# Performance work log

Measured on AMD Instinct MI355X. Metric: run time of the kernel, lower is better.

The kernel has to match this reference:

```python
import jax, jax.numpy as jnp
import numpy as np

MARGIN_POS = 0.0
MARGIN_NEG = 1.0
NUM_CLASSES = 1000


def setup_inputs() -> dict:
    key = jax.random.key(0)
    k1, k2, k3, k4, k5 = jax.random.split(key, 5)
    B, D, M = 1024, 512, 32768
    R = M - B  # memory bank length after dedup/truncate
    embeddings = jax.random.normal(k1, (B, D), dtype=jnp.float32)
    labels = jax.random.randint(k2, (B,), 0, NUM_CLASSES).astype(jnp.int64)
    emb_mem = jax.random.normal(k3, (R, D), dtype=jnp.float32)
    # offset so memory labels are disjoint from batch labels (torch.isin dedup is a no-op)
    lbl_mem = (jax.random.randint(k4, (R,), 0, NUM_CLASSES) + NUM_CLASSES).astype(jnp.int64)
    add_to_mem = jax.random.randint(k5, (B,), 0, 2).astype(bool)
    return {"embeddings": embeddings, "labels": labels, "emb_mem": emb_mem,
            "lbl_mem": lbl_mem, "add_to_mem": add_to_mem}


def _loss(embeddings, labels, emb_mem, lbl_mem):
    B = embeddings.shape[0]
    # reference set = detached batch embeddings ++ memory bank (both are constants w.r.t. grad)
    ref_e = jax.lax.stop_gradient(jnp.concatenate([embeddings, emb_mem], axis=0))  # [R, D]
    ref_l = jnp.concatenate([labels, lbl_mem], axis=0)                              # [R]
    idx_ref = jnp.concatenate([jnp.arange(B, dtype=labels.dtype),
                               -jnp.ones(lbl_mem.shape[0], dtype=labels.dtype)])    # [R]
    # squared L2 distance matrix [B, R] via (|a|^2 + |b|^2 - 2 a.b), clamped at 0
    sq_a = jnp.sum(embeddings * embeddings, axis=1)  # [B]
    sq_b = jnp.sum(ref_e * ref_e, axis=1)            # [R]
    d = jnp.maximum(sq_a[:, None] + sq_b[None, :] - 2.0 * (embeddings @ ref_e.T), 0.0)
    not_self = idx_ref[None, :] != jnp.arange(B, dtype=labels.dtype)[:, None]  # [B, R]
    same = labels[:, None] == ref_l[None, :]                                   # [B, R]
    loss_ap = d - MARGIN_POS
    loss_an = jnp.maximum(MARGIN_NEG - d, 0.0)
    mask_pos = same & not_self & (loss_ap > 0)
    mask_neg = (~same) & not_self & (loss_an > 0)
    eps = 1e-6
    loss_pos = (jnp.where(mask_pos, loss_ap, 0.0).sum(1)
                / (mask_pos.sum(1).astype(d.dtype) + eps)).sum()
    loss_neg = (jnp.where(mask_neg, loss_an, 0.0).sum(1)
                / (mask_neg.sum(1).astype(d.dtype) + eps)).sum()
    return (loss_pos + loss_neg) / B


def reference(embeddings, labels, emb_mem, lbl_mem, add_to_mem):
    # add_to_mem only affects the (stateful) memory-bank update, not the returned loss
    return _loss(embeddings, labels, emb_mem, lbl_mem)
```

## Files before the change

kernel.cpp:

```cpp
#include <hip/hip_runtime.h>

typedef __attribute__((ext_vector_type(8))) short short8;
typedef __attribute__((ext_vector_type(4))) float f32x4;

#define GLOAD16(g, l)                                                        \
  __builtin_amdgcn_global_load_lds(                                          \
      (const __attribute__((address_space(1))) unsigned int*)(g),            \
      (__attribute__((address_space(3))) unsigned int*)(l), 16, 0, 0)

__device__ __forceinline__ unsigned short f2bf(float f) {
  union { float f; unsigned int u; } v;
  v.f = f;
  unsigned int u = v.u;
  u += 0x7FFFu + ((u >> 16) & 1u);
  return (unsigned short)(u >> 16);
}

__device__ __forceinline__ short8 pack8(float4 a, float4 b) {
  short8 r;
  r[0] = (short)f2bf(a.x); r[1] = (short)f2bf(a.y);
  r[2] = (short)f2bf(a.z); r[3] = (short)f2bf(a.w);
  r[4] = (short)f2bf(b.x); r[5] = (short)f2bf(b.y);
  r[6] = (short)f2bf(b.z); r[7] = (short)f2bf(b.w);
  return r;
}

#define BM 128
#define BN 128
#define BK 32

__global__ __launch_bounds__(256)
void prep2_kernel(const float* __restrict__ emb, const int* __restrict__ labels,
                  const float* __restrict__ emb_mem, const int* __restrict__ lbl_mem,
                  unsigned short* __restrict__ refbf, float* __restrict__ sqb,
                  int* __restrict__ reflab, float* __restrict__ facc,
                  int* __restrict__ fcnt, int Bn, int Dn, int Mn) {
  if (blockIdx.x == 0 && threadIdx.x == 0) { *facc = 0.f; *fcnt = 0; }
  int wid = threadIdx.x >> 6, lane = threadIdx.x & 63;
  int row = blockIdx.x * 4 + wid;
  if (row >= Mn) return;
  const float* src = (row < Bn) ? (emb + (size_t)row * Dn)
                                : (emb_mem + (size_t)(row - Bn) * Dn);
  unsigned short* dst = refbf + (size_t)row * Dn;
  float s = 0.f;
  for (int c0 = lane * 8; c0 < Dn; c0 += 64 * 8) {
    float4 v0 = ((const float4*)(src + c0))[0];
    float4 v1 = ((const float4*)(src + c0))[1];
    s += v0.x * v0.x + v0.y * v0.y + v0.z * v0.z + v0.w * v0.w;
    s += v1.x * v1.x + v1.y * v1.y + v1.z * v1.z + v1.w * v1.w;
    *(short8*)(dst + c0) = pack8(v0, v1);
  }
#pragma unroll
  for (int off = 32; off; off >>= 1) s += __shfl_xor(s, off);
  if (lane == 0) {
    sqb[row] = s;
    reflab[row] = (row < Bn) ? labels[row] : lbl_mem[row - Bn];
  }
}

__global__ __launch_bounds__(256)
void gemm512_kernel(const unsigned short* __restrict__ refbf,
                    const float* __restrict__ sqb,
                    const int* __restrict__ reflab,
                    float* __restrict__ part) {
  __shared__ __align__(16) char smem[32768];
  unsigned short* As = (unsigned short*)smem;
  unsigned short* Bs = (unsigned short*)(smem + 8192);
  f32x4* red4 = (f32x4*)smem;

  const int ntiles = 256;
  int bid = blockIdx.x;
  int c = bid & 7, g = bid >> 3;
  int jt = c * 32 + (g >> 3);
  int it = g & 7;
  int rowBase = it * BM, colBase = jt * BN;

  int tid = threadIdx.x, lane = tid & 63, w = tid >> 6;
  int wr = w >> 1, wc = w & 1;
  int l16 = lane & 15, quad = lane >> 4;
  int lrow = lane >> 2, lk = lane & 3;
  int r0 = w * 32 + lrow;
  int ca = (lk - (r0 >> 1)) & 3;

  const char* gA0 = (const char*)refbf + (size_t)(rowBase + r0) * 1024 + ca * 16;
  const char* gA1 = gA0 + 16 * 1024;
  const char* gB0 = (const char*)refbf + (size_t)(colBase + r0) * 1024 + ca * 16;
  const char* gB1 = gB0 + 16 * 1024;
  char* lA = (char*)As + w * 2048;
  char* lB = (char*)Bs + w * 2048;

  f32x4 acc[4][4] = {};
#pragma unroll
  for (int kk = 0; kk < 16; ++kk) {
    GLOAD16(gA0 + kk * 64, lA);
    GLOAD16(gA1 + kk * 64, lA + 1024);
    GLOAD16(gB0 + kk * 64, lB);
    GLOAD16(gB1 + kk * 64, lB + 1024);
    __syncthreads();
    short8 af[4], bfr[4];
#pragma unroll
    for (int mi = 0; mi < 4; ++mi) {
      int row = wr * 64 + mi * 16 + l16;
      af[mi] = *(const short8*)&As[row * BK + ((quad + (row >> 1)) & 3) * 8];
    }
#pragma unroll
    for (int ni = 0; ni < 4; ++ni) {
      int row = wc * 64 + ni * 16 + l16;
      bfr[ni] = *(const short8*)&Bs[row * BK + ((quad + (row >> 1)) & 3) * 8];
    }
#pragma unroll
    for (int mi = 0; mi < 4; ++mi)
#pragma unroll
      for (int ni = 0; ni < 4; ++ni)
        acc[mi][ni] = __builtin_amdgcn_mfma_f32_16x16x32_bf16(
            af[mi], bfr[ni], acc[mi][ni], 0, 0, 0);
    __syncthreads();
  }

  float sqc[4];
  int labc[4];
#pragma unroll
  for (int ni = 0; ni < 4; ++ni) {
    int gcol = colBase + wc * 64 + ni * 16 + l16;
    sqc[ni] = sqb[gcol];
    labc[ni] = reflab[gcol];
  }
#pragma unroll
  for (int mi = 0; mi < 4; ++mi) {
    int lr0 = wr * 64 + mi * 16 + quad * 4;
#pragma unroll
    for (int r = 0; r < 4; ++r) {
      int lrl = lr0 + r;
      int grow = rowBase + lrl;
      float sqr = sqb[grow];
      int labr = reflab[grow];
      float ps = 0.f, ns = 0.f, cpk = 0.f;
#pragma unroll
      for (int ni = 0; ni < 4; ++ni) {
        int gcol = colBase + wc * 64 + ni * 16 + l16;
        float dist = fmaxf(sqr + sqc[ni] - 2.0f * acc[mi][ni][r], 0.f);
        bool self = (gcol == grow);
        bool same = (labc[ni] == labr);
        if (same && !self && dist > 0.f) { ps += dist; cpk += 1.f; }
        if (!same && !self && dist < 1.f) { ns += 1.f - dist; cpk += 512.f; }
      }
      ps += __shfl_xor(ps, 8);
      ns += __shfl_xor(ns, 8);
      cpk += __shfl_xor(cpk, 8);
      if (l16 < 8) {
        f32x4 v = {ps, ns, cpk, 0.f};
        red4[(wc * BM + lrl) * 8 + l16] = v;
      }
    }
  }
  __syncthreads();
  if (tid < BM) {
    f32x4 s = {0.f, 0.f, 0.f, 0.f};
#pragma unroll
    for (int c2 = 0; c2 < 2; ++c2)
#pragma unroll
      for (int k = 0; k < 8; ++k)
        s += red4[(c2 * BM + tid) * 8 + ((k + tid) & 7)];
    float nc = floorf(s[2] * (1.0f / 512.0f));
    float pc = s[2] - 512.f * nc;
    f32x4 o = {s[0], pc, s[1], nc};
    ((f32x4*)part)[(size_t)(rowBase + tid) * ntiles + jt] = o;
  }
}

__global__ __launch_bounds__(256)
void gemm_generic_kernel(const unsigned short* __restrict__ refbf,
                         const float* __restrict__ sqb,
                         const int* __restrict__ reflab,
                         float* __restrict__ part,
                         int Dn, int mtiles, int ntiles) {
  __shared__ unsigned short As[BM * BK];
  __shared__ unsigned short Bs[BN * BK];
  __shared__ f32x4 redbuf4[2 * BM];

  int bid = blockIdx.x;
  int it = bid % mtiles, jt = bid / mtiles;
  int rowBase = it * BM, colBase = jt * BN;
  int tid = threadIdx.x, lane = tid & 63, w = tid >> 6;
  int wr = w >> 1, wc = w & 1;
  int l16 = lane & 15, quad = lane >> 4;
  int lrow = lane >> 2, lk = lane & 3;
  size_t rowB = (size_t)Dn * 2;
  int r0 = w * 32 + lrow;
  int ca = (lk - (r0 >> 1)) & 3;
  const char* gA0 = (const char*)refbf + (size_t)(rowBase + r0) * rowB + ca * 16;
  const char* gA1 = gA0 + 16 * rowB;
  const char* gB0 = (const char*)refbf + (size_t)(colBase + r0) * rowB + ca * 16;
  const char* gB1 = gB0 + 16 * rowB;
  char* lA = (char*)As + w * 2048;
  char* lB = (char*)Bs + w * 2048;

  f32x4 acc[4][4] = {};
  for (int k0 = 0; k0 < Dn; k0 += BK) {
    int koff = k0 * 2;
    GLOAD16(gA0 + koff, lA);
    GLOAD16(gA1 + koff, lA + 1024);
    GLOAD16(gB0 + koff, lB);
    GLOAD16(gB1 + koff, lB + 1024);
    __syncthreads();
    short8 af[4], bfr[4];
#pragma unroll
    for (int mi = 0; mi < 4; ++mi) {
      int row = wr * 64 + mi * 16 + l16;
      af[mi] = *(const short8*)&As[row * BK + ((quad + (row >> 1)) & 3) * 8];
    }
#pragma unroll
    for (int ni = 0; ni < 4; ++ni) {
      int row = wc * 64 + ni * 16 + l16;
      bfr[ni] = *(const short8*)&Bs[row * BK + ((quad + (row >> 1)) & 3) * 8];
    }
#pragma unroll
    for (int mi = 0; mi < 4; ++mi)
#pragma unroll
      for (int ni = 0; ni < 4; ++ni)
        acc[mi][ni] = __builtin_amdgcn_mfma_f32_16x16x32_bf16(
            af[mi], bfr[ni], acc[mi][ni], 0, 0, 0);
    __syncthreads();
  }

  float sqc[4];
  int labc[4];
#pragma unroll
  for (int ni = 0; ni < 4; ++ni) {
    int gcol = colBase + wc * 64 + ni * 16 + l16;
    sqc[ni] = sqb[gcol];
    labc[ni] = reflab[gcol];
  }
#pragma unroll
  for (int mi = 0; mi < 4; ++mi) {
    int lr0 = wr * 64 + mi * 16 + quad * 4;
#pragma unroll
    for (int r = 0; r < 4; ++r) {
      int lrl = lr0 + r;
      int grow = rowBase + lrl;
      float sqr = sqb[grow];
      int labr = reflab[grow];
      float ps = 0.f, pc = 0.f, ns = 0.f, nc = 0.f;
#pragma unroll
      for (int ni = 0; ni < 4; ++ni) {
        int gcol = colBase + wc * 64 + ni * 16 + l16;
        float dist = fmaxf(sqr + sqc[ni] - 2.0f * acc[mi][ni][r], 0.f);
        bool self = (gcol == grow);
        bool same = (labc[ni] == labr);
        if (same && !self && dist > 0.f) { ps += dist; pc += 1.f; }
        if (!same && !self && dist < 1.f) { ns += 1.f - dist; nc += 1.f; }
      }
#pragma unroll
      for (int off = 8; off; off >>= 1) {
        ps += __shfl_xor(ps, off);
        pc += __shfl_xor(pc, off);
        ns += __shfl_xor(ns, off);
        nc += __shfl_xor(nc, off);
      }
      if (l16 == 0) {
        f32x4 v = {ps, pc, ns, nc};
        redbuf4[wc * BM + lrl] = v;
      }
    }
  }
  __syncthreads();
  if (tid < BM) {
    f32x4 s = redbuf4[tid] + redbuf4[BM + tid];
    ((f32x4*)part)[(size_t)(rowBase + tid) * ntiles + jt] = s;
  }
}

__global__ __launch_bounds__(256)
void reduce_final_kernel(const float* __restrict__ part,
                         float* __restrict__ facc, int* __restrict__ fcnt,
                         float* __restrict__ out, int Bn, int ntiles) {
  __shared__ float rsum[4];
  int tid = threadIdx.x, w = tid >> 6, lane = tid & 63;
  int row = blockIdx.x * 4 + w;
  const f32x4* part4 = (const f32x4*)part;
  float rl = 0.f;
  if (row < Bn) {
    f32x4 a = {0.f, 0.f, 0.f, 0.f};
    for (int j = lane; j < ntiles; j += 64)
      a += part4[(size_t)row * ntiles + j];
#pragma unroll
    for (int off = 32; off; off >>= 1) {
      a[0] += __shfl_xor(a[0], off);
      a[1] += __shfl_xor(a[1], off);
      a[2] += __shfl_xor(a[2], off);
      a[3] += __shfl_xor(a[3], off);
    }
    rl = a[0] / (a[1] + 1e-6f) + a[2] / (a[3] + 1e-6f);
  }
  if (lane == 0) rsum[w] = rl;
  __syncthreads();
  if (tid == 0) {
    float bs = rsum[0] + rsum[1] + rsum[2] + rsum[3];
    atomicAdd(facc, bs);
    __threadfence();
    int old = atomicAdd(fcnt, 1);
    if (old == (int)gridDim.x - 1) {
      __threadfence();
      float tot = atomicAdd(facc, 0.f);
      out[0] = tot / (float)Bn;
    }
  }
}

extern "C" void kernel_launch(void* const* d_in, const int* in_sizes, int n_in,
                              void* d_out, int out_size, void* d_ws, size_t ws_size,
                              hipStream_t stream) {
  const float* emb     = (const float*)d_in[0];
  const int*   labels  = (const int*)d_in[1];
  const float* emb_mem = (const float*)d_in[2];
  const int*   lbl_mem = (const int*)d_in[3];

  int Bn = in_sizes[1];
  int Dn = in_sizes[0] / Bn;
  int Rn = in_sizes[3];
  int Mn = Bn + Rn;
  int mtiles = Bn / BM, ntiles = Mn / BN;

  char* ws = (char*)d_ws;
  unsigned short* refbf = (unsigned short*)ws;
  size_t off = (size_t)Mn * Dn * 2;
  float* sqb    = (float*)(ws + off);
  int*   reflab = (int*)(ws + off + (size_t)Mn * 4);
  float* part   = (float*)(ws + off + (size_t)Mn * 8);
  float* facc   = part + (size_t)Bn * ntiles * 4;
  int*   fcnt   = (int*)(facc + 1);

  prep2_kernel<<<(Mn + 3) / 4, 256, 0, stream>>>(
      emb, labels, emb_mem, lbl_mem, refbf, sqb, reflab, facc, fcnt, Bn, Dn, Mn);

  if (Dn == 512 && mtiles == 8 && ntiles == 256) {
    gemm512_kernel<<<2048, 256, 0, stream>>>(refbf, sqb, reflab, part);
  } else {
    gemm_generic_kernel<<<mtiles * ntiles, 256, 0, stream>>>(
        refbf, sqb, reflab, part, Dn, mtiles, ntiles);
  }

  reduce_final_kernel<<<(Bn + 3) / 4, 256, 0, stream>>>(
      part, facc, fcnt, (float*)d_out, Bn, ntiles);
}
```

Measured before the change: 164.0 us.

## Load GEMM fragments directly from global into registers with double buffering

The 512-dim GEMM kernel no longer stages A/B tiles through LDS with global_load_lds and two barriers per k-step. Each lane now loads its MFMA fragments straight from global memory into registers, prefetching the next k-slice while the current one feeds the MFMAs, and launch bounds request 3 blocks per CU. This removes the LDS round-trip and the barriers. In exchange every wave re-reads shared rows from global/L2 with no intra-block reuse, and register pressure goes up.

```diff
diff --git a/kernel.cpp b/kernel.cpp
--- a/kernel.cpp
+++ b/kernel.cpp
@@ -58,15 +58,12 @@
   }
 }
 
-__global__ __launch_bounds__(256)
-void gemm512_kernel(const unsigned short* __restrict__ refbf,
-                    const float* __restrict__ sqb,
-                    const int* __restrict__ reflab,
-                    float* __restrict__ part) {
-  __shared__ __align__(16) char smem[32768];
-  unsigned short* As = (unsigned short*)smem;
-  unsigned short* Bs = (unsigned short*)(smem + 8192);
-  f32x4* red4 = (f32x4*)smem;
+__global__ __launch_bounds__(256, 3)
+void gemm512r_kernel(const unsigned short* __restrict__ refbf,
+                     const float* __restrict__ sqb,
+                     const int* __restrict__ reflab,
+                     float* __restrict__ part) {
+  __shared__ f32x4 red4[2 * BM * 8];
 
   const int ntiles = 256;
   int bid = blockIdx.x;
@@ -78,43 +75,41 @@
   int tid = threadIdx.x, lane = tid & 63, w = tid >> 6;
   int wr = w >> 1, wc = w & 1;
   int l16 = lane & 15, quad = lane >> 4;
-  int lrow = lane >> 2, lk = lane & 3;
-  int r0 = w * 32 + lrow;
-  int ca = (lk - (r0 >> 1)) & 3;
-
-  const char* gA0 = (const char*)refbf + (size_t)(rowBase + r0) * 1024 + ca * 16;
-  const char* gA1 = gA0 + 16 * 1024;
-  const char* gB0 = (const char*)refbf + (size_t)(colBase + r0) * 1024 + ca * 16;
-  const char* gB1 = gB0 + 16 * 1024;
-  char* lA = (char*)As + w * 2048;
-  char* lB = (char*)Bs + w * 2048;
+
+  const char* aP[4];
+  const char* bP[4];
+#pragma unroll
+  for (int mi = 0; mi < 4; ++mi)
+    aP[mi] = (const char*)refbf +
+             (size_t)(rowBase + wr * 64 + mi * 16 + l16) * 1024 + quad * 16;
+#pragma unroll
+  for (int ni = 0; ni < 4; ++ni)
+    bP[ni] = (const char*)refbf +
+             (size_t)(colBase + wc * 64 + ni * 16 + l16) * 1024 + quad * 16;
 
   f32x4 acc[4][4] = {};
+  short8 af[2][4], bfr[2][4];
+#pragma unroll
+  for (int mi = 0; mi < 4; ++mi) af[0][mi] = *(const short8*)(aP[mi]);
+#pragma unroll
+  for (int ni = 0; ni < 4; ++ni) bfr[0][ni] = *(const short8*)(bP[ni]);
+
 #pragma unroll
   for (int kk = 0; kk < 16; ++kk) {
-    GLOAD16(gA0 + kk * 64, lA);
-    GLOAD16(gA1 + kk * 64, lA + 1024);
-    GLOAD16(gB0 + kk * 64, lB);
-    GLOAD16(gB1 + kk * 64, lB + 1024);
-    __syncthreads();
-    short8 af[4], bfr[4];
-#pragma unroll
-    for (int mi = 0; mi < 4; ++mi) {
-      int row = wr * 64 + mi * 16 + l16;
-      af[mi] = *(const short8*)&As[row * BK + ((quad + (row >> 1)) & 3) * 8];
-    }
-#pragma unroll
-    for (int ni = 0; ni < 4; ++ni) {
-      int row = wc * 64 + ni * 16 + l16;
-      bfr[ni] = *(const short8*)&Bs[row * BK + ((quad + (row >> 1)) & 3) * 8];
+    int cur = kk & 1, nxt = cur ^ 1;
+    if (kk < 15) {
+      int ko = (kk + 1) * 64;
+#pragma unroll
+      for (int mi = 0; mi < 4; ++mi) af[nxt][mi] = *(const short8*)(aP[mi] + ko);
+#pragma unroll
+      for (int ni = 0; ni < 4; ++ni) bfr[nxt][ni] = *(const short8*)(bP[ni] + ko);
     }
 #pragma unroll
     for (int mi = 0; mi < 4; ++mi)
 #pragma unroll
       for (int ni = 0; ni < 4; ++ni)
         acc[mi][ni] = __builtin_amdgcn_mfma_f32_16x16x32_bf16(
-            af[mi], bfr[ni], acc[mi][ni], 0, 0, 0);
-    __syncthreads();
+            af[cur][mi], bfr[cur][ni], acc[mi][ni], 0, 0, 0);
   }
 
   float sqc[4];
@@ -334,7 +329,7 @@
       emb, labels, emb_mem, lbl_mem, refbf, sqb, reflab, facc, fcnt, Bn, Dn, Mn);
 
   if (Dn == 512 && mtiles == 8 && ntiles == 256) {
-    gemm512_kernel<<<2048, 256, 0, stream>>>(refbf, sqb, reflab, part);
+    gemm512r_kernel<<<2048, 256, 0, stream>>>(refbf, sqb, reflab, part);
   } else {
     gemm_generic_kernel<<<mtiles * ntiles, 256, 0, stream>>>(
         refbf, sqb, reflab, part, Dn, mtiles, ntiles);
```

Result: slower. 242.6 us (+47.9%).

## Fuse prep, GEMM and reduction into one cooperative persistent kernel

Applied to the files above, without the earlier changes.

Replaces the three separate launches (bf16 convert/norms, distance GEMM with masked partial sums, final reduction) with one cooperative kernel of 512 persistent blocks. The phases are separated by grid-wide syncs, and each block loops over rows and GEMM tiles. This removes launch overhead and inter-kernel gaps. In exchange it adds grid-sync costs, loses the oversubscribed 2048-block GEMM grid, and keeps the three-kernel path as a fallback if the cooperative launch fails.

```diff
diff --git a/kernel.cpp b/kernel.cpp
--- a/kernel.cpp
+++ b/kernel.cpp
@@ -1,4 +1,7 @@
 #include <hip/hip_runtime.h>
+#include <hip/hip_cooperative_groups.h>
+
+namespace cg = cooperative_groups;
 
 typedef __attribute__((ext_vector_type(8))) short short8;
 typedef __attribute__((ext_vector_type(4))) float f32x4;
@@ -28,6 +31,180 @@
 #define BM 128
 #define BN 128
 #define BK 32
+
+__global__ __launch_bounds__(256, 2)
+void fused512_kernel(const float* __restrict__ emb, const int* __restrict__ labels,
+                     const float* __restrict__ emb_mem, const int* __restrict__ lbl_mem,
+                     unsigned short* __restrict__ refbf, float* __restrict__ sqb,
+                     int* __restrict__ reflab, float* __restrict__ part,
+                     float* __restrict__ rowloss, float* __restrict__ out,
+                     int Bn, int Mn) {
+  __shared__ __align__(16) char smem[32768];
+  unsigned short* As = (unsigned short*)smem;
+  unsigned short* Bs = (unsigned short*)(smem + 8192);
+  f32x4* red4 = (f32x4*)smem;
+
+  cg::grid_group grid = cg::this_grid();
+  const int Dn = 512, ntiles = 256;
+  int tid = threadIdx.x, lane = tid & 63, w = tid >> 6;
+  int bid = blockIdx.x, G = gridDim.x;
+
+  for (int row = bid * 4 + w; row < Mn; row += G * 4) {
+    const float* src = (row < Bn) ? (emb + (size_t)row * Dn)
+                                  : (emb_mem + (size_t)(row - Bn) * Dn);
+    unsigned short* dst = refbf + (size_t)row * Dn;
+    float s = 0.f;
+    {
+      int c0 = lane * 8;
+      float4 v0 = ((const float4*)(src + c0))[0];
+      float4 v1 = ((const float4*)(src + c0))[1];
+      s += v0.x * v0.x + v0.y * v0.y + v0.z * v0.z + v0.w * v0.w;
+      s += v1.x * v1.x + v1.y * v1.y + v1.z * v1.z + v1.w * v1.w;
+      *(short8*)(dst + c0) = pack8(v0, v1);
+    }
+#pragma unroll
+    for (int off = 32; off; off >>= 1) s += __shfl_xor(s, off);
+    if (lane == 0) {
+      sqb[row] = s;
+      reflab[row] = (row < Bn) ? labels[row] : lbl_mem[row - Bn];
+    }
+  }
+  __threadfence();
+  grid.sync();
+
+  int wr = w >> 1, wc = w & 1;
+  int l16 = lane & 15, quad = lane >> 4;
+  int lrow = lane >> 2, lk = lane & 3;
+  int sr0 = w * 32 + lrow;
+  int ca = (lk - (sr0 >> 1)) & 3;
+  char* lA = (char*)As + w * 2048;
+  char* lB = (char*)Bs + w * 2048;
+
+  for (int t = bid; t < 2048; t += G) {
+    int c = t & 7, g = t >> 3;
+    int jt = c * 32 + (g >> 3);
+    int it = g & 7;
+    int rowBase = it * BM, colBase = jt * BN;
+
+    const char* gA0 = (const char*)refbf + (size_t)(rowBase + sr0) * 1024 + ca * 16;
+    const char* gA1 = gA0 + 16 * 1024;
+    const char* gB0 = (const char*)refbf + (size_t)(colBase + sr0) * 1024 + ca * 16;
+    const char* gB1 = gB0 + 16 * 1024;
+
+    f32x4 acc[4][4] = {};
+#pragma unroll
+    for (int kk = 0; kk < 16; ++kk) {
+      GLOAD16(gA0 + kk * 64, lA);
+      GLOAD16(gA1 + kk * 64, lA + 1024);
+      GLOAD16(gB0 + kk * 64, lB);
+      GLOAD16(gB1 + kk * 64, lB + 1024);
+      __syncthreads();
+      short8 af[4], bfr[4];
+#pragma unroll
+      for (int mi = 0; mi < 4; ++mi) {
+        int row = wr * 64 + mi * 16 + l16;
+        af[mi] = *(const short8*)&As[row * BK + ((quad + (row >> 1)) & 3) * 8];
+      }
+#pragma unroll
+      for (int ni = 0; ni < 4; ++ni) {
+        int row = wc * 64 + ni * 16 + l16;
+        bfr[ni] = *(const short8*)&Bs[row * BK + ((quad + (row >> 1)) & 3) * 8];
+      }
+#pragma unroll
+      for (int mi = 0; mi < 4; ++mi)
+#pragma unroll
+        for (int ni = 0; ni < 4; ++ni)
+          acc[mi][ni] = __builtin_amdgcn_mfma_f32_16x16x32_bf16(
+              af[mi], bfr[ni], acc[mi][ni], 0, 0, 0);
+      __syncthreads();
+    }
+
+    float sqc[4];
+    int labc[4];
+#pragma unroll
+    for (int ni = 0; ni < 4; ++ni) {
+      int gcol = colBase + wc * 64 + ni * 16 + l16;
+      sqc[ni] = sqb[gcol];
+      labc[ni] = reflab[gcol];
+    }
+#pragma unroll
+    for (int mi = 0; mi < 4; ++mi) {
+      int lr0 = wr * 64 + mi * 16 + quad * 4;
+#pragma unroll
+      for (int r = 0; r < 4; ++r) {
+        int lrl = lr0 + r;
+        int grow = rowBase + lrl;
+        float sqr = sqb[grow];
+        int labr = reflab[grow];
+        float ps = 0.f, ns = 0.f, cpk = 0.f;
+#pragma unroll
+        for (int ni = 0; ni < 4; ++ni) {
+          int gcol = colBase + wc * 64 + ni * 16 + l16;
+          float dist = fmaxf(sqr + sqc[ni] - 2.0f * acc[mi][ni][r], 0.f);
+          bool self = (gcol == grow);
+          bool same = (labc[ni] == labr);
+          if (same && !self && dist > 0.f) { ps += dist; cpk += 1.f; }
+          if (!same && !self && dist < 1.f) { ns += 1.f - dist; cpk += 512.f; }
+        }
+        ps += __shfl_xor(ps, 8);
+        ns += __shfl_xor(ns, 8);
+        cpk += __shfl_xor(cpk, 8);
+        if (l16 < 8) {
+          f32x4 v = {ps, ns, cpk, 0.f};
+          red4[(wc * BM + lrl) * 8 + l16] = v;
+        }
+      }
+    }
+    __syncthreads();
+    if (tid < BM) {
+      f32x4 s = {0.f, 0.f, 0.f, 0.f};
+#pragma unroll
+      for (int c2 = 0; c2 < 2; ++c2)
+#pragma unroll
+        for (int k = 0; k < 8; ++k)
+          s += red4[(c2 * BM + tid) * 8 + ((k + tid) & 7)];
+      float nc = floorf(s[2] * (1.0f / 512.0f));
+      float pc = s[2] - 512.f * nc;
+      f32x4 o = {s[0], pc, s[1], nc};
+      ((f32x4*)part)[(size_t)(rowBase + tid) * ntiles + jt] = o;
+    }
+    __syncthreads();
+  }
+  __threadfence();
+  grid.sync();
+
+  const f32x4* part4 = (const f32x4*)part;
+  for (int gr = bid; gr < Bn; gr += G) {
+    f32x4 a = part4[(size_t)gr * ntiles + tid];
+#pragma unroll
+    for (int off = 32; off; off >>= 1) {
+      a[0] += __shfl_xor(a[0], off);
+      a[1] += __shfl_xor(a[1], off);
+      a[2] += __shfl_xor(a[2], off);
+      a[3] += __shfl_xor(a[3], off);
+    }
+    if (lane == 0) red4[w] = a;
+    __syncthreads();
+    if (tid == 0) {
+      f32x4 s = red4[0] + red4[1] + red4[2] + red4[3];
+      rowloss[gr] = s[0] / (s[1] + 1e-6f) + s[2] / (s[3] + 1e-6f);
+    }
+    __syncthreads();
+  }
+  __threadfence();
+  grid.sync();
+
+  if (bid == 0) {
+    float v = 0.f;
+    for (int i = tid; i < Bn; i += 256) v += rowloss[i];
+#pragma unroll
+    for (int off = 32; off; off >>= 1) v += __shfl_xor(v, off);
+    float* rs = (float*)smem;
+    if (lane == 0) rs[w] = v;
+    __syncthreads();
+    if (tid == 0) out[0] = (rs[0] + rs[1] + rs[2] + rs[3]) / (float)Bn;
+  }
+}
 
 __global__ __launch_bounds__(256)
 void prep2_kernel(const float* __restrict__ emb, const int* __restrict__ labels,
@@ -59,116 +236,6 @@
 }
 
 __global__ __launch_bounds__(256)
-void gemm512_kernel(const unsigned short* __restrict__ refbf,
-                    const float* __restrict__ sqb,
-                    const int* __restrict__ reflab,
-                    float* __restrict__ part) {
-  __shared__ __align__(16) char smem[32768];
-  unsigned short* As = (unsigned short*)smem;
-  unsigned short* Bs = (unsigned short*)(smem + 8192);
-  f32x4* red4 = (f32x4*)smem;
-
-  const int ntiles = 256;
-  int bid = blockIdx.x;
-  int c = bid & 7, g = bid >> 3;
-  int jt = c * 32 + (g >> 3);
-  int it = g & 7;
-  int rowBase = it * BM, colBase = jt * BN;
-
-  int tid = threadIdx.x, lane = tid & 63, w = tid >> 6;
-  int wr = w >> 1, wc = w & 1;
-  int l16 = lane & 15, quad = lane >> 4;
-  int lrow = lane >> 2, lk = lane & 3;
-  int r0 = w * 32 + lrow;
-  int ca = (lk - (r0 >> 1)) & 3;
-
-  const char* gA0 = (const char*)refbf + (size_t)(rowBase + r0) * 1024 + ca * 16;
-  const char* gA1 = gA0 + 16 * 1024;
-  const char* gB0 = (const char*)refbf + (size_t)(colBase + r0) * 1024 + ca * 16;
-  const char* gB1 = gB0 + 16 * 1024;
-  char* lA = (char*)As + w * 2048;
-  char* lB = (char*)Bs + w * 2048;
-
-  f32x4 acc[4][4] = {};
-#pragma unroll
-  for (int kk = 0; kk < 16; ++kk) {
-    GLOAD16(gA0 + kk * 64, lA);
-    GLOAD16(gA1 + kk * 64, lA + 1024);
-    GLOAD16(gB0 + kk * 64, lB);
-    GLOAD16(gB1 + kk * 64, lB + 1024);
-    __syncthreads();
-    short8 af[4], bfr[4];
-#pragma unroll
-    for (int mi = 0; mi < 4; ++mi) {
-      int row = wr * 64 + mi * 16 + l16;
-      af[mi] = *(const short8*)&As[row * BK + ((quad + (row >> 1)) & 3) * 8];
-    }
-#pragma unroll
-    for (int ni = 0; ni < 4; ++ni) {
-      int row = wc * 64 + ni * 16 + l16;
-      bfr[ni] = *(const short8*)&Bs[row * BK + ((quad + (row >> 1)) & 3) * 8];
-    }
-#pragma unroll
-    for (int mi = 0; mi < 4; ++mi)
-#pragma unroll
-      for (int ni = 0; ni < 4; ++ni)
-        acc[mi][ni] = __builtin_amdgcn_mfma_f32_16x16x32_bf16(
-            af[mi], bfr[ni], acc[mi][ni], 0, 0, 0);
-    __syncthreads();
-  }
-
-  float sqc[4];
-  int labc[4];
-#pragma unroll
-  for (int ni = 0; ni < 4; ++ni) {
-    int gcol = colBase + wc * 64 + ni * 16 + l16;
-    sqc[ni] = sqb[gcol];
-    labc[ni] = reflab[gcol];
-  }
-#pragma unroll
-  for (int mi = 0; mi < 4; ++mi) {
-    int lr0 = wr * 64 + mi * 16 + quad * 4;
-#pragma unroll
-    for (int r = 0; r < 4; ++r) {
-      int lrl = lr0 + r;
-      int grow = rowBase + lrl;
-      float sqr = sqb[grow];
-      int labr = reflab[grow];
-      float ps = 0.f, ns = 0.f, cpk = 0.f;
-#pragma unroll
-      for (int ni = 0; ni < 4; ++ni) {
-        int gcol = colBase + wc * 64 + ni * 16 + l16;
-        float dist = fmaxf(sqr + sqc[ni] - 2.0f * acc[mi][ni][r], 0.f);
-        bool self = (gcol == grow);
-        bool same = (labc[ni] == labr);
-        if (same && !self && dist > 0.f) { ps += dist; cpk += 1.f; }
-        if (!same && !self && dist < 1.f) { ns += 1.f - dist; cpk += 512.f; }
-      }
-      ps += __shfl_xor(ps, 8);
-      ns += __shfl_xor(ns, 8);
-      cpk += __shfl_xor(cpk, 8);
-      if (l16 < 8) {
-        f32x4 v = {ps, ns, cpk, 0.f};
-        red4[(wc * BM + lrl) * 8 + l16] = v;
-      }
-    }
-  }
-  __syncthreads();
-  if (tid < BM) {
-    f32x4 s = {0.f, 0.f, 0.f, 0.f};
-#pragma unroll
-    for (int c2 = 0; c2 < 2; ++c2)
-#pragma unroll
-      for (int k = 0; k < 8; ++k)
-        s += red4[(c2 * BM + tid) * 8 + ((k + tid) & 7)];
-    float nc = floorf(s[2] * (1.0f / 512.0f));
-    float pc = s[2] - 512.f * nc;
-    f32x4 o = {s[0], pc, s[1], nc};
-    ((f32x4*)part)[(size_t)(rowBase + tid) * ntiles + jt] = o;
-  }
-}
-
-__global__ __launch_bounds__(256)
 void gemm_generic_kernel(const unsigned short* __restrict__ refbf,
                          const float* __restrict__ sqb,
                          const int* __restrict__ reflab,
@@ -324,22 +391,28 @@
   char* ws = (char*)d_ws;
   unsigned short* refbf = (unsigned short*)ws;
   size_t off = (size_t)Mn * Dn * 2;
-  float* sqb    = (float*)(ws + off);
-  int*   reflab = (int*)(ws + off + (size_t)Mn * 4);
-  float* part   = (float*)(ws + off + (size_t)Mn * 8);
-  float* facc   = part + (size_t)Bn * ntiles * 4;
-  int*   fcnt   = (int*)(facc + 1);
-
-  prep2_kernel<<<(Mn + 3) / 4, 256, 0, stream>>>(
-      emb, labels, emb_mem, lbl_mem, refbf, sqb, reflab, facc, fcnt, Bn, Dn, Mn);
-
-  if (Dn == 512 && mtiles == 8 && ntiles == 256) {
-    gemm512_kernel<<<2048, 256, 0, stream>>>(refbf, sqb, reflab, part);
-  } else {
+  float* sqb     = (float*)(ws + off);
+  int*   reflab  = (int*)(ws + off + (size_t)Mn * 4);
+  float* part    = (float*)(ws + off + (size_t)Mn * 8);
+  float* rowloss = part + (size_t)Bn * ntiles * 4;
+  float* facc    = rowloss + Bn;
+  int*   fcnt    = (int*)(facc + 1);
+  float* outp    = (float*)d_out;
+
+  bool fast = (Dn == 512 && mtiles == 8 && ntiles == 256);
+  hipError_t cerr = hipErrorUnknown;
+  if (fast) {
+    void* args[] = {&emb, &labels, &emb_mem, &lbl_mem, &refbf, &sqb, &reflab,
+                    &part, &rowloss, &outp, &Bn, &Mn};
+    cerr = hipLaunchCooperativeKernel((void*)fused512_kernel, dim3(512),
+                                      dim3(256), args, 0, stream);
+  }
+  if (cerr != hipSuccess) {
+    prep2_kernel<<<(Mn + 3) / 4, 256, 0, stream>>>(
+        emb, labels, emb_mem, lbl_mem, refbf, sqb, reflab, facc, fcnt, Bn, Dn, Mn);
     gemm_generic_kernel<<<mtiles * ntiles, 256, 0, stream>>>(
         refbf, sqb, reflab, part, Dn, mtiles, ntiles);
-  }
-
-  reduce_final_kernel<<<(Bn + 3) / 4, 256, 0, stream>>>(
-      part, facc, fcnt, (float*)d_out, Bn, ntiles);
-}
+    reduce_final_kernel<<<(Bn + 3) / 4, 256, 0, stream>>>(
+        part, facc, fcnt, (float*)d_out, Bn, ntiles);
+  }
+}
```

Measured after the change: 505.9 us. +208.5%, slower.

## Widen GEMM tile to 128x256 and process four rows per wave in prep

Applied to the files above, without the earlier changes.

The fused distance/loss GEMM now computes a 128x256 output tile per block, so each wave holds 4x8 accumulators and the grid has half as many blocks. This raises MFMA work per loaded A fragment and halves the partial-sum array that the final reduction reads. The prep kernel now has each wave convert four rows at once to expose more outstanding loads. The costs are higher register pressure (launch bounds of 2 blocks per CU) and fewer blocks to fill the GPU.

```diff
diff --git a/kernel.cpp b/kernel.cpp
--- a/kernel.cpp
+++ b/kernel.cpp
@@ -30,98 +30,127 @@
 #define BK 32
 
 __global__ __launch_bounds__(256)
-void prep2_kernel(const float* __restrict__ emb, const int* __restrict__ labels,
+void prep3_kernel(const float* __restrict__ emb, const int* __restrict__ labels,
                   const float* __restrict__ emb_mem, const int* __restrict__ lbl_mem,
                   unsigned short* __restrict__ refbf, float* __restrict__ sqb,
                   int* __restrict__ reflab, float* __restrict__ facc,
                   int* __restrict__ fcnt, int Bn, int Dn, int Mn) {
   if (blockIdx.x == 0 && threadIdx.x == 0) { *facc = 0.f; *fcnt = 0; }
-  int wid = threadIdx.x >> 6, lane = threadIdx.x & 63;
-  int row = blockIdx.x * 4 + wid;
-  if (row >= Mn) return;
-  const float* src = (row < Bn) ? (emb + (size_t)row * Dn)
-                                : (emb_mem + (size_t)(row - Bn) * Dn);
-  unsigned short* dst = refbf + (size_t)row * Dn;
-  float s = 0.f;
+  int w = threadIdx.x >> 6, lane = threadIdx.x & 63;
+  int base = (blockIdx.x * 4 + w) * 4;
+  const float* src[4];
+  bool ok[4];
+#pragma unroll
+  for (int i = 0; i < 4; ++i) {
+    int row = base + i;
+    ok[i] = row < Mn;
+    src[i] = !ok[i] ? emb
+             : (row < Bn) ? (emb + (size_t)row * Dn)
+                          : (emb_mem + (size_t)(row - Bn) * Dn);
+  }
+  float s[4] = {0.f, 0.f, 0.f, 0.f};
   for (int c0 = lane * 8; c0 < Dn; c0 += 64 * 8) {
-    float4 v0 = ((const float4*)(src + c0))[0];
-    float4 v1 = ((const float4*)(src + c0))[1];
-    s += v0.x * v0.x + v0.y * v0.y + v0.z * v0.z + v0.w * v0.w;
-    s += v1.x * v1.x + v1.y * v1.y + v1.z * v1.z + v1.w * v1.w;
-    *(short8*)(dst + c0) = pack8(v0, v1);
-  }
-#pragma unroll
-  for (int off = 32; off; off >>= 1) s += __shfl_xor(s, off);
+    float4 a0[4], a1[4];
+#pragma unroll
+    for (int i = 0; i < 4; ++i) {
+      a0[i] = ((const float4*)(src[i] + c0))[0];
+      a1[i] = ((const float4*)(src[i] + c0))[1];
+    }
+#pragma unroll
+    for (int i = 0; i < 4; ++i) {
+      s[i] += a0[i].x * a0[i].x + a0[i].y * a0[i].y + a0[i].z * a0[i].z +
+              a0[i].w * a0[i].w + a1[i].x * a1[i].x + a1[i].y * a1[i].y +
+              a1[i].z * a1[i].z + a1[i].w * a1[i].w;
+      if (ok[i]) *(short8*)(refbf + (size_t)(base + i) * Dn + c0) = pack8(a0[i], a1[i]);
+    }
+  }
+#pragma unroll
+  for (int off = 32; off; off >>= 1) {
+#pragma unroll
+    for (int i = 0; i < 4; ++i) s[i] += __shfl_xor(s[i], off);
+  }
   if (lane == 0) {
-    sqb[row] = s;
-    reflab[row] = (row < Bn) ? labels[row] : lbl_mem[row - Bn];
-  }
-}
-
-__global__ __launch_bounds__(256)
-void gemm512_kernel(const unsigned short* __restrict__ refbf,
-                    const float* __restrict__ sqb,
-                    const int* __restrict__ reflab,
-                    float* __restrict__ part) {
+#pragma unroll
+    for (int i = 0; i < 4; ++i) {
+      int row = base + i;
+      if (ok[i]) {
+        sqb[row] = s[i];
+        reflab[row] = (row < Bn) ? labels[row] : lbl_mem[row - Bn];
+      }
+    }
+  }
+}
+
+__global__ __launch_bounds__(256, 2)
+void gemm512x2_kernel(const unsigned short* __restrict__ refbf,
+                      const float* __restrict__ sqb,
+                      const int* __restrict__ reflab,
+                      float* __restrict__ part) {
   __shared__ __align__(16) char smem[32768];
   unsigned short* As = (unsigned short*)smem;
   unsigned short* Bs = (unsigned short*)(smem + 8192);
   f32x4* red4 = (f32x4*)smem;
 
-  const int ntiles = 256;
+  const int npart = 128;
   int bid = blockIdx.x;
   int c = bid & 7, g = bid >> 3;
-  int jt = c * 32 + (g >> 3);
+  int jp = c * 16 + (g >> 3);
   int it = g & 7;
-  int rowBase = it * BM, colBase = jt * BN;
+  int rowBase = it * BM, colBase = jp * 256;
 
   int tid = threadIdx.x, lane = tid & 63, w = tid >> 6;
   int wr = w >> 1, wc = w & 1;
   int l16 = lane & 15, quad = lane >> 4;
   int lrow = lane >> 2, lk = lane & 3;
-  int r0 = w * 32 + lrow;
-  int ca = (lk - (r0 >> 1)) & 3;
-
-  const char* gA0 = (const char*)refbf + (size_t)(rowBase + r0) * 1024 + ca * 16;
+
+  int ra = w * 32 + lrow;
+  int caa = (lk - (ra >> 1)) & 3;
+  const char* gA0 = (const char*)refbf + (size_t)(rowBase + ra) * 1024 + caa * 16;
   const char* gA1 = gA0 + 16 * 1024;
-  const char* gB0 = (const char*)refbf + (size_t)(colBase + r0) * 1024 + ca * 16;
+  char* lA = (char*)As + w * 2048;
+  int rb = w * 64 + lrow;
+  int cab = (lk - (rb >> 1)) & 3;
+  const char* gB0 = (const char*)refbf + (size_t)(colBase + rb) * 1024 + cab * 16;
   const char* gB1 = gB0 + 16 * 1024;
-  char* lA = (char*)As + w * 2048;
-  char* lB = (char*)Bs + w * 2048;
-
-  f32x4 acc[4][4] = {};
-#pragma unroll
+  const char* gB2 = gB0 + 32 * 1024;
+  const char* gB3 = gB0 + 48 * 1024;
+  char* lB = (char*)Bs + w * 4096;
+
+  f32x4 acc[4][8] = {};
   for (int kk = 0; kk < 16; ++kk) {
-    GLOAD16(gA0 + kk * 64, lA);
-    GLOAD16(gA1 + kk * 64, lA + 1024);
-    GLOAD16(gB0 + kk * 64, lB);
-    GLOAD16(gB1 + kk * 64, lB + 1024);
+    int ko = kk * 64;
+    GLOAD16(gA0 + ko, lA);
+    GLOAD16(gA1 + ko, lA + 1024);
+    GLOAD16(gB0 + ko, lB);
+    GLOAD16(gB1 + ko, lB + 1024);
+    GLOAD16(gB2 + ko, lB + 2048);
+    GLOAD16(gB3 + ko, lB + 3072);
     __syncthreads();
-    short8 af[4], bfr[4];
+    short8 af[4], bfr[8];
 #pragma unroll
     for (int mi = 0; mi < 4; ++mi) {
       int row = wr * 64 + mi * 16 + l16;
       af[mi] = *(const short8*)&As[row * BK + ((quad + (row >> 1)) & 3) * 8];
     }
 #pragma unroll
-    for (int ni = 0; ni < 4; ++ni) {
-      int row = wc * 64 + ni * 16 + l16;
+    for (int ni = 0; ni < 8; ++ni) {
+      int row = wc * 128 + ni * 16 + l16;
       bfr[ni] = *(const short8*)&Bs[row * BK + ((quad + (row >> 1)) & 3) * 8];
     }
 #pragma unroll
     for (int mi = 0; mi < 4; ++mi)
 #pragma unroll
-      for (int ni = 0; ni < 4; ++ni)
+      for (int ni = 0; ni < 8; ++ni)
         acc[mi][ni] = __builtin_amdgcn_mfma_f32_16x16x32_bf16(
             af[mi], bfr[ni], acc[mi][ni], 0, 0, 0);
     __syncthreads();
   }
 
-  float sqc[4];
-  int labc[4];
-#pragma unroll
-  for (int ni = 0; ni < 4; ++ni) {
-    int gcol = colBase + wc * 64 + ni * 16 + l16;
+  float sqc[8];
+  int labc[8];
+#pragma unroll
+  for (int ni = 0; ni < 8; ++ni) {
+    int gcol = colBase + wc * 128 + ni * 16 + l16;
     sqc[ni] = sqb[gcol];
     labc[ni] = reflab[gcol];
   }
@@ -136,8 +165,8 @@
       int labr = reflab[grow];
       float ps = 0.f, ns = 0.f, cpk = 0.f;
 #pragma unroll
-      for (int ni = 0; ni < 4; ++ni) {
-        int gcol = colBase + wc * 64 + ni * 16 + l16;
+      for (int ni = 0; ni < 8; ++ni) {
+        int gcol = colBase + wc * 128 + ni * 16 + l16;
         float dist = fmaxf(sqr + sqc[ni] - 2.0f * acc[mi][ni][r], 0.f);
         bool self = (gcol == grow);
         bool same = (labc[ni] == labr);
@@ -164,7 +193,7 @@
     float nc = floorf(s[2] * (1.0f / 512.0f));
     float pc = s[2] - 512.f * nc;
     f32x4 o = {s[0], pc, s[1], nc};
-    ((f32x4*)part)[(size_t)(rowBase + tid) * ntiles + jt] = o;
+    ((f32x4*)part)[(size_t)(rowBase + tid) * npart + jp] = o;
   }
 }
 
@@ -273,7 +302,7 @@
 __global__ __launch_bounds__(256)
 void reduce_final_kernel(const float* __restrict__ part,
                          float* __restrict__ facc, int* __restrict__ fcnt,
-                         float* __restrict__ out, int Bn, int ntiles) {
+                         float* __restrict__ out, int Bn, int npart) {
   __shared__ float rsum[4];
   int tid = threadIdx.x, w = tid >> 6, lane = tid & 63;
   int row = blockIdx.x * 4 + w;
@@ -281,8 +310,8 @@
   float rl = 0.f;
   if (row < Bn) {
     f32x4 a = {0.f, 0.f, 0.f, 0.f};
-    for (int j = lane; j < ntiles; j += 64)
-      a += part4[(size_t)row * ntiles + j];
+    for (int j = lane; j < npart; j += 64)
+      a += part4[(size_t)row * npart + j];
 #pragma unroll
     for (int off = 32; off; off >>= 1) {
       a[0] += __shfl_xor(a[0], off);
@@ -330,16 +359,18 @@
   float* facc   = part + (size_t)Bn * ntiles * 4;
   int*   fcnt   = (int*)(facc + 1);
 
-  prep2_kernel<<<(Mn + 3) / 4, 256, 0, stream>>>(
+  prep3_kernel<<<(Mn + 15) / 16, 256, 0, stream>>>(
       emb, labels, emb_mem, lbl_mem, refbf, sqb, reflab, facc, fcnt, Bn, Dn, Mn);
 
-  if (Dn == 512 && mtiles == 8 && ntiles == 256) {
-    gemm512_kernel<<<2048, 256, 0, stream>>>(refbf, sqb, reflab, part);
+  bool fast = (Dn == 512 && mtiles == 8 && ntiles == 256);
+  if (fast) {
+    gemm512x2_kernel<<<1024, 256, 0, stream>>>(refbf, sqb, reflab, part);
+    reduce_final_kernel<<<(Bn + 3) / 4, 256, 0, stream>>>(
+        part, facc, fcnt, (float*)d_out, Bn, 128);
   } else {
     gemm_generic_kernel<<<mtiles * ntiles, 256, 0, stream>>>(
         refbf, sqb, reflab, part, Dn, mtiles, ntiles);
-  }
-
-  reduce_final_kernel<<<(Bn + 3) / 4, 256, 0, stream>>>(
-      part, facc, fcnt, (float*)d_out, Bn, ntiles);
-}
+    reduce_final_kernel<<<(Bn + 3) / 4, 256, 0, stream>>>(
+        part, facc, fcnt, (float*)d_out, Bn, ntiles);
+  }
+}
```

After: 162.9 us. Within noise of the previous version (-0.7%).
